# Kernel optimization log

Measured on AMD Instinct MI355X. Metric: run time of the kernel, lower is better.

## Reference

```python
import jax, jax.numpy as jnp
import numpy as np

BN_EPS = 1e-5


def _gin_layer(x, src, dst, n_nodes, W1, b1, W2, b2, gamma, beta):
    # GINConv with eps=0: z_i = x_i + sum_{(j->i) in E} x_j, then 2-layer MLP
    agg = jax.ops.segment_sum(x[src], dst, num_segments=n_nodes)  # [N, d]
    z = x + agg
    z = jax.nn.relu(z @ W1 + b1) @ W2 + b2
    # BatchNorm1d (training mode: biased batch statistics over node dim)
    mean = jnp.mean(z, axis=0)
    var = jnp.var(z, axis=0)
    z = (z - mean) * jax.lax.rsqrt(var + BN_EPS) * gamma + beta
    return jax.nn.relu(z)  # dropout p=0 -> identity


def setup_inputs() -> dict:
    key = jax.random.key(0)
    ks = jax.random.split(key, 8)
    N, E, D, L = 50000, 800000, 128, 2
    h = jax.random.normal(ks[0], (N, D), dtype=jnp.float32)
    edge_index = jax.random.randint(ks[1], (2, E), 0, N, dtype=jnp.int64)
    scale = 1.0 / np.sqrt(D)
    W1 = jax.random.normal(ks[2], (L, D, D), dtype=jnp.float32) * scale
    b1 = jax.random.normal(ks[3], (L, D), dtype=jnp.float32) * 0.01
    W2 = jax.random.normal(ks[4], (L, D, D), dtype=jnp.float32) * scale
    b2 = jax.random.normal(ks[5], (L, D), dtype=jnp.float32) * 0.01
    gamma = jnp.ones((L, D), dtype=jnp.float32)
    beta = jnp.zeros((L, D), dtype=jnp.float32)
    return {"h": h, "edge_index": edge_index, "W1": W1, "b1": b1,
            "W2": W2, "b2": b2, "gamma": gamma, "beta": beta}


def reference(h, edge_index, W1, b1, W2, b2, gamma, beta):
    src, dst = edge_index[0], edge_index[1]
    n_nodes = h.shape[0]
    n_layers = W1.shape[0]
    outs = []
    x = h
    for i in range(n_layers):
        x = _gin_layer(x, src, dst, n_nodes, W1[i], b1[i], W2[i], b2[i], gamma[i], beta[i])
        outs.append(x)
    return jnp.stack(outs)  # [L, N, D] == hs[1:]
```

## Files before the change

kernel.cpp:

```cpp
#include <hip/hip_runtime.h>

#define D 128
#define BN_EPS 1e-5f

typedef __attribute__((ext_vector_type(8))) short short8;
typedef __attribute__((ext_vector_type(4))) float f32x4;

__device__ inline unsigned short f2bf(float f) {
    union { float f; unsigned int u; } v; v.f = f;
    unsigned int u = v.u;
    unsigned int r = (u + 0x7FFFu + ((u >> 16) & 1u)) >> 16;
    return (unsigned short)r;
}

__device__ inline float bfbits2f(unsigned int bits) {
    union { unsigned int u; float f; } v; v.u = bits;
    return v.f;
}

__device__ inline float4 bf2f4(uint2 v) {
    float4 r;
    r.x = bfbits2f(v.x << 16);
    r.y = bfbits2f(v.x & 0xFFFF0000u);
    r.z = bfbits2f(v.y << 16);
    r.w = bfbits2f(v.y & 0xFFFF0000u);
    return r;
}

__global__ void hist_dst(const int* __restrict__ dst, int* __restrict__ cnt, int E) {
    int e = blockIdx.x * blockDim.x + threadIdx.x;
    if (e < E) atomicAdd(&cnt[dst[e]], 1);
}

__global__ void reduce_cnt(const int* __restrict__ cnt, int* __restrict__ bsum, int n) {
    __shared__ int s[256];
    int tid = threadIdx.x;
    int i = blockIdx.x * 256 + tid;
    s[tid] = (i < n) ? cnt[i] : 0;
    __syncthreads();
    for (int ofs = 128; ofs > 0; ofs >>= 1) {
        if (tid < ofs) s[tid] += s[tid + ofs];
        __syncthreads();
    }
    if (tid == 0) bsum[blockIdx.x] = s[0];
}

__global__ void scan_bsums(const int* __restrict__ bsum, int* __restrict__ blockOff,
                           int* __restrict__ offN, int nb) {
    __shared__ int s[256];
    int tid = threadIdx.x;
    int v = (tid < nb) ? bsum[tid] : 0;
    s[tid] = v;
    __syncthreads();
    for (int ofs = 1; ofs < 256; ofs <<= 1) {
        int t = (tid >= ofs) ? s[tid - ofs] : 0;
        __syncthreads();
        s[tid] += t;
        __syncthreads();
    }
    if (tid < nb) blockOff[tid] = s[tid] - v;
    if (tid == nb - 1) *offN = s[tid];
}

__global__ void scan_partial(const int* __restrict__ cnt, int* __restrict__ off,
                             int* __restrict__ cursor, const int* __restrict__ blockOff, int n) {
    __shared__ int s[256];
    int tid = threadIdx.x;
    int i = blockIdx.x * 256 + tid;
    int v = (i < n) ? cnt[i] : 0;
    s[tid] = v;
    __syncthreads();
    for (int ofs = 1; ofs < 256; ofs <<= 1) {
        int t = (tid >= ofs) ? s[tid - ofs] : 0;
        __syncthreads();
        s[tid] += t;
        __syncthreads();
    }
    if (i < n) {
        int o = blockOff[blockIdx.x] + s[tid] - v;
        off[i] = o;
        cursor[i] = o;
    }
}

__global__ void fill_csr(const int* __restrict__ src, const int* __restrict__ dst,
                         int* __restrict__ cursor, int* __restrict__ eidx, int E) {
    int e = blockIdx.x * blockDim.x + threadIdx.x;
    if (e >= E) return;
    int d = dst[e];
    int pos = atomicAdd(&cursor[d], 1);
    eidx[pos] = src[e];
}

__global__ void wprep(const float* __restrict__ W1, const float* __restrict__ W2,
                      unsigned short* __restrict__ Wt, int L) {
    int idx = blockIdx.x * 256 + threadIdx.x;
    int m = idx >> 14;
    int rem = idx & 16383;
    int c = rem >> 7, k = rem & 127;
    const float* W = (m < L) ? (W1 + (size_t)m * D * D) : (W2 + (size_t)(m - L) * D * D);
    Wt[(size_t)m * D * D + c * D + k] = f2bf(W[k * D + c]);
}

__global__ void x2bf(const float* __restrict__ x, unsigned short* __restrict__ xb, int n8) {
    int i = blockIdx.x * 256 + threadIdx.x;
    if (i >= n8) return;
    float4 a = reinterpret_cast<const float4*>(x)[2 * i];
    float4 b = reinterpret_cast<const float4*>(x)[2 * i + 1];
    uint4 o;
    o.x = (unsigned)f2bf(a.x) | ((unsigned)f2bf(a.y) << 16);
    o.y = (unsigned)f2bf(a.z) | ((unsigned)f2bf(a.w) << 16);
    o.z = (unsigned)f2bf(b.x) | ((unsigned)f2bf(b.y) << 16);
    o.w = (unsigned)f2bf(b.z) | ((unsigned)f2bf(b.w) << 16);
    reinterpret_cast<uint4*>(xb)[i] = o;
}

__global__ __launch_bounds__(256) void gather_bf(
        const unsigned short* __restrict__ xb, const int* __restrict__ off,
        const int* __restrict__ eidx, unsigned short* __restrict__ zb, int N) {
    int t = blockIdx.x * blockDim.x + threadIdx.x;
    int node = t >> 5;
    if (node >= N) return;
    int lane = t & 31;
    int beg = off[node], end = off[node + 1];
    float4 acc = bf2f4(*reinterpret_cast<const uint2*>(xb + (size_t)node * D + lane * 4));
    int e = beg;
    for (; e + 2 <= end; e += 2) {
        int s0 = eidx[e], s1 = eidx[e + 1];
        uint2 v0 = *reinterpret_cast<const uint2*>(xb + (size_t)s0 * D + lane * 4);
        uint2 v1 = *reinterpret_cast<const uint2*>(xb + (size_t)s1 * D + lane * 4);
        float4 f0 = bf2f4(v0), f1 = bf2f4(v1);
        acc.x += f0.x + f1.x; acc.y += f0.y + f1.y;
        acc.z += f0.z + f1.z; acc.w += f0.w + f1.w;
    }
    if (e < end) {
        int s0 = eidx[e];
        float4 f0 = bf2f4(*reinterpret_cast<const uint2*>(xb + (size_t)s0 * D + lane * 4));
        acc.x += f0.x; acc.y += f0.y; acc.z += f0.z; acc.w += f0.w;
    }
    uint2 o;
    o.x = (unsigned)f2bf(acc.x) | ((unsigned)f2bf(acc.y) << 16);
    o.y = (unsigned)f2bf(acc.z) | ((unsigned)f2bf(acc.w) << 16);
    *reinterpret_cast<uint2*>(zb + (size_t)node * D + lane * 4) = o;
}

__global__ __launch_bounds__(256) void gemm1_mfma(
        const unsigned short* __restrict__ A, const unsigned short* __restrict__ Wt,
        const float* __restrict__ bias, unsigned short* __restrict__ Out, int N) {
    __shared__ __align__(16) char sW[32768];
    const int tid = threadIdx.x;
    #pragma unroll
    for (int it = 0; it < 8; it++) {
        int idx = tid + it * 256;
        int row = idx >> 4, slot = idx & 15;
        uint4 v = *reinterpret_cast<const uint4*>(Wt + ((size_t)idx << 3));
        *reinterpret_cast<uint4*>(sW + row * 256 + ((slot * 16) ^ ((row & 7) << 4))) = v;
    }
    __syncthreads();

    const int lane = tid & 63, wv = tid >> 6;
    const int r0 = blockIdx.x * 64 + wv * 16;
    int arow = r0 + (lane & 15); if (arow >= N) arow = N - 1;
    const unsigned short* aptr = A + (size_t)arow * D + ((lane >> 4) << 3);

    f32x4 acc[8];
    #pragma unroll
    for (int ct = 0; ct < 8; ct++) {
        float b = bias[ct * 16 + (lane & 15)];
        acc[ct] = (f32x4){b, b, b, b};
    }
    #pragma unroll
    for (int ks = 0; ks < 4; ks++) {
        short8 a = *reinterpret_cast<const short8*>(aptr + ks * 32);
        #pragma unroll
        for (int ct = 0; ct < 8; ct++) {
            int rr = ct * 16 + (lane & 15);
            int kb = ks * 64 + ((lane >> 4) << 4);
            short8 bfr = *reinterpret_cast<const short8*>(sW + rr * 256 + (kb ^ ((rr & 7) << 4)));
            acc[ct] = __builtin_amdgcn_mfma_f32_16x16x32_bf16(a, bfr, acc[ct], 0, 0, 0);
        }
    }
    #pragma unroll
    for (int ct = 0; ct < 8; ct++) {
        #pragma unroll
        for (int r = 0; r < 4; r++) {
            int row = r0 + ((lane >> 4) << 2) + r;
            if (row < N)
                Out[(size_t)row * D + ct * 16 + (lane & 15)] = f2bf(fmaxf(acc[ct][r], 0.f));
        }
    }
}

__global__ __launch_bounds__(256) void gemm2_mfma(
        const unsigned short* __restrict__ A, const unsigned short* __restrict__ Wt,
        const float* __restrict__ bias, float* __restrict__ Out,
        float* __restrict__ gstats, int N) {
    __shared__ __align__(16) char sW[32768];
    __shared__ float sStat[2 * D];
    const int tid = threadIdx.x;
    if (tid < 2 * D) sStat[tid] = 0.f;
    #pragma unroll
    for (int it = 0; it < 8; it++) {
        int idx = tid + it * 256;
        int row = idx >> 4, slot = idx & 15;
        uint4 v = *reinterpret_cast<const uint4*>(Wt + ((size_t)idx << 3));
        *reinterpret_cast<uint4*>(sW + row * 256 + ((slot * 16) ^ ((row & 7) << 4))) = v;
    }
    __syncthreads();

    const int lane = tid & 63, wv = tid >> 6;
    const int r0 = blockIdx.x * 64 + wv * 16;
    int arow = r0 + (lane & 15); if (arow >= N) arow = N - 1;
    const unsigned short* aptr = A + (size_t)arow * D + ((lane >> 4) << 3);

    f32x4 acc[8];
    #pragma unroll
    for (int ct = 0; ct < 8; ct++) {
        float b = bias[ct * 16 + (lane & 15)];
        acc[ct] = (f32x4){b, b, b, b};
    }
    #pragma unroll
    for (int ks = 0; ks < 4; ks++) {
        short8 a = *reinterpret_cast<const short8*>(aptr + ks * 32);
        #pragma unroll
        for (int ct = 0; ct < 8; ct++) {
            int rr = ct * 16 + (lane & 15);
            int kb = ks * 64 + ((lane >> 4) << 4);
            short8 bfr = *reinterpret_cast<const short8*>(sW + rr * 256 + (kb ^ ((rr & 7) << 4)));
            acc[ct] = __builtin_amdgcn_mfma_f32_16x16x32_bf16(a, bfr, acc[ct], 0, 0, 0);
        }
    }
    #pragma unroll
    for (int ct = 0; ct < 8; ct++) {
        float s = 0.f, q = 0.f;
        #pragma unroll
        for (int r = 0; r < 4; r++) {
            int row = r0 + ((lane >> 4) << 2) + r;
            float v = acc[ct][r];
            if (row < N) {
                Out[(size_t)row * D + ct * 16 + (lane & 15)] = v;
                s += v; q += v * v;
            }
        }
        s += __shfl_xor(s, 16); q += __shfl_xor(q, 16);
        s += __shfl_xor(s, 32); q += __shfl_xor(q, 32);
        if (lane < 16) {
            atomicAdd(&sStat[ct * 16 + lane], s);
            atomicAdd(&sStat[D + ct * 16 + lane], q);
        }
    }
    __syncthreads();
    if (tid < 2 * D) atomicAdd(&gstats[tid], sStat[tid]);
}

__global__ void bn_relu_bf(float* __restrict__ y, unsigned short* __restrict__ xb,
                           const float* __restrict__ stats,
                           const float* __restrict__ gamma, const float* __restrict__ beta,
                           int N) {
    int i = blockIdx.x * blockDim.x + threadIdx.x;
    int n4 = N * D / 4;
    if (i >= n4) return;
    int c0 = (i << 2) & (D - 1);
    float4 v = reinterpret_cast<float4*>(y)[i];
    float o[4] = {v.x, v.y, v.z, v.w};
    float invN = 1.0f / (float)N;
    #pragma unroll
    for (int j = 0; j < 4; j++) {
        int c = c0 + j;
        float mean = stats[c] * invN;
        float var  = stats[D + c] * invN - mean * mean;
        float sc = rsqrtf(var + BN_EPS) * gamma[c];
        float t = (o[j] - mean) * sc + beta[c];
        o[j] = fmaxf(t, 0.f);
    }
    float4 r; r.x = o[0]; r.y = o[1]; r.z = o[2]; r.w = o[3];
    reinterpret_cast<float4*>(y)[i] = r;
    uint2 ob;
    ob.x = (unsigned)f2bf(o[0]) | ((unsigned)f2bf(o[1]) << 16);
    ob.y = (unsigned)f2bf(o[2]) | ((unsigned)f2bf(o[3]) << 16);
    reinterpret_cast<uint2*>(xb)[i] = ob;
}

extern "C" void kernel_launch(void* const* d_in, const int* in_sizes, int n_in,
                              void* d_out, int out_size, void* d_ws, size_t ws_size,
                              hipStream_t stream) {
    const float* h     = (const float*)d_in[0];
    const int*   ei    = (const int*)d_in[1];
    const float* W1    = (const float*)d_in[2];
    const float* b1    = (const float*)d_in[3];
    const float* W2    = (const float*)d_in[4];
    const float* b2    = (const float*)d_in[5];
    const float* gamma = (const float*)d_in[6];
    const float* beta  = (const float*)d_in[7];
    float* out = (float*)d_out;

    const int N = in_sizes[0] / D;
    const int E = in_sizes[1] / 2;
    const int L = in_sizes[2] / (D * D);
    const int nb = (N + 255) / 256;

    unsigned short* zb  = (unsigned short*)d_ws;
    unsigned short* xb  = zb + (size_t)N * D;
    unsigned short* Wt  = xb + (size_t)N * D;
    float* stats = (float*)(Wt + (size_t)2 * L * D * D);
    int* cnt      = (int*)(stats + (size_t)L * 2 * D);
    int* off      = cnt + N;
    int* cursor   = off + N + 1;
    int* bsum     = cursor + N;
    int* blockOff = bsum + nb;
    int* eidx     = blockOff + nb;

    const int* src = ei;
    const int* dst = ei + E;

    const int n4 = N * D / 4;
    const int n8 = N * D / 8;
    const int ewBlocks = (E + 255) / 256;
    const int gatherBlocks = (N * 32 + 255) / 256;
    const int gemmBlocks = (N + 63) / 64;
    const int bnBlocks = (n4 + 255) / 256;
    const int wprepBlocks = (2 * L * D * D) / 256;

    hipMemsetAsync(cnt, 0, N * sizeof(int), stream);
    hipMemsetAsync(stats, 0, (size_t)L * 2 * D * sizeof(float), stream);
    wprep<<<wprepBlocks, 256, 0, stream>>>(W1, W2, Wt, L);
    x2bf<<<(n8 + 255) / 256, 256, 0, stream>>>(h, xb, n8);

    hist_dst<<<ewBlocks, 256, 0, stream>>>(dst, cnt, E);
    reduce_cnt<<<nb, 256, 0, stream>>>(cnt, bsum, N);
    scan_bsums<<<1, 256, 0, stream>>>(bsum, blockOff, off + N, nb);
    scan_partial<<<nb, 256, 0, stream>>>(cnt, off, cursor, blockOff, N);
    fill_csr<<<ewBlocks, 256, 0, stream>>>(src, dst, cursor, eidx, E);

    for (int l = 0; l < L; l++) {
        float* y = out + (size_t)l * N * D;

        gather_bf<<<gatherBlocks, 256, 0, stream>>>(xb, off, eidx, zb, N);
        gemm1_mfma<<<gemmBlocks, 256, 0, stream>>>(zb, Wt + (size_t)l * D * D,
                                                   b1 + (size_t)l * D, zb, N);
        gemm2_mfma<<<gemmBlocks, 256, 0, stream>>>(zb, Wt + (size_t)(L + l) * D * D,
                                                   b2 + (size_t)l * D, y, stats + (size_t)l * 2 * D, N);
        bn_relu_bf<<<bnBlocks, 256, 0, stream>>>(y, xb, stats + (size_t)l * 2 * D,
                                                 gamma + (size_t)l * D, beta + (size_t)l * D, N);
    }
}
```

Baseline: 276.5 us.

## Record edge ranks during histogram and read GEMM weights directly from global memory

The histogram kernel now records each edge's atomic rank, so the CSR fill no longer needs a second pass of atomics on a cursor array and instead writes to off[dst]+rank. Both MFMA GEMM kernels drop the per-block LDS staging of the weight matrix. They read B fragments straight from global memory (served by cache) and process 32 rows per wave instead of 16, which reuses each B fragment across two MFMAs. This removes the shared-memory fill and barrier, halves the block count and raises register use. It also adds an E-sized rank buffer to the workspace.

```diff
diff --git a/kernel.cpp b/kernel.cpp
--- a/kernel.cpp
+++ b/kernel.cpp
@@ -27,9 +27,11 @@
     return r;
 }
 
-__global__ void hist_dst(const int* __restrict__ dst, int* __restrict__ cnt, int E) {
+__global__ void hist_rank(const int* __restrict__ dst, int* __restrict__ cnt,
+                          int* __restrict__ rank, int E) {
     int e = blockIdx.x * blockDim.x + threadIdx.x;
-    if (e < E) atomicAdd(&cnt[dst[e]], 1);
+    if (e >= E) return;
+    rank[e] = atomicAdd(&cnt[dst[e]], 1);
 }
 
 __global__ void reduce_cnt(const int* __restrict__ cnt, int* __restrict__ bsum, int n) {
@@ -63,7 +65,7 @@
 }
 
 __global__ void scan_partial(const int* __restrict__ cnt, int* __restrict__ off,
-                             int* __restrict__ cursor, const int* __restrict__ blockOff, int n) {
+                             const int* __restrict__ blockOff, int n) {
     __shared__ int s[256];
     int tid = threadIdx.x;
     int i = blockIdx.x * 256 + tid;
@@ -76,20 +78,15 @@
         s[tid] += t;
         __syncthreads();
     }
-    if (i < n) {
-        int o = blockOff[blockIdx.x] + s[tid] - v;
-        off[i] = o;
-        cursor[i] = o;
-    }
-}
-
-__global__ void fill_csr(const int* __restrict__ src, const int* __restrict__ dst,
-                         int* __restrict__ cursor, int* __restrict__ eidx, int E) {
+    if (i < n) off[i] = blockOff[blockIdx.x] + s[tid] - v;
+}
+
+__global__ void fill2(const int* __restrict__ src, const int* __restrict__ dst,
+                      const int* __restrict__ rank, const int* __restrict__ off,
+                      int* __restrict__ eidx, int E) {
     int e = blockIdx.x * blockDim.x + threadIdx.x;
     if (e >= E) return;
-    int d = dst[e];
-    int pos = atomicAdd(&cursor[d], 1);
-    eidx[pos] = src[e];
+    eidx[off[dst[e]] + rank[e]] = src[e];
 }
 
 __global__ void wprep(const float* __restrict__ W1, const float* __restrict__ W2,
@@ -147,46 +144,46 @@
 __global__ __launch_bounds__(256) void gemm1_mfma(
         const unsigned short* __restrict__ A, const unsigned short* __restrict__ Wt,
         const float* __restrict__ bias, unsigned short* __restrict__ Out, int N) {
-    __shared__ __align__(16) char sW[32768];
     const int tid = threadIdx.x;
-    #pragma unroll
-    for (int it = 0; it < 8; it++) {
-        int idx = tid + it * 256;
-        int row = idx >> 4, slot = idx & 15;
-        uint4 v = *reinterpret_cast<const uint4*>(Wt + ((size_t)idx << 3));
-        *reinterpret_cast<uint4*>(sW + row * 256 + ((slot * 16) ^ ((row & 7) << 4))) = v;
-    }
-    __syncthreads();
-
     const int lane = tid & 63, wv = tid >> 6;
-    const int r0 = blockIdx.x * 64 + wv * 16;
-    int arow = r0 + (lane & 15); if (arow >= N) arow = N - 1;
-    const unsigned short* aptr = A + (size_t)arow * D + ((lane >> 4) << 3);
-
-    f32x4 acc[8];
+    const int r0 = blockIdx.x * 128 + wv * 32;
+    const int koff = (lane >> 4) << 3;
+    const int col = lane & 15;
+
+    int ar0 = r0 + col;       if (ar0 >= N) ar0 = N - 1;
+    int ar1 = r0 + 16 + col;  if (ar1 >= N) ar1 = N - 1;
+    const unsigned short* ap0 = A + (size_t)ar0 * D + koff;
+    const unsigned short* ap1 = A + (size_t)ar1 * D + koff;
+    const unsigned short* wp  = Wt + (size_t)col * D + koff;
+
+    f32x4 acc[2][8];
     #pragma unroll
     for (int ct = 0; ct < 8; ct++) {
-        float b = bias[ct * 16 + (lane & 15)];
-        acc[ct] = (f32x4){b, b, b, b};
+        float b = bias[ct * 16 + col];
+        acc[0][ct] = (f32x4){b, b, b, b};
+        acc[1][ct] = (f32x4){b, b, b, b};
     }
     #pragma unroll
     for (int ks = 0; ks < 4; ks++) {
-        short8 a = *reinterpret_cast<const short8*>(aptr + ks * 32);
+        short8 a0 = *reinterpret_cast<const short8*>(ap0 + ks * 32);
+        short8 a1 = *reinterpret_cast<const short8*>(ap1 + ks * 32);
         #pragma unroll
         for (int ct = 0; ct < 8; ct++) {
-            int rr = ct * 16 + (lane & 15);
-            int kb = ks * 64 + ((lane >> 4) << 4);
-            short8 bfr = *reinterpret_cast<const short8*>(sW + rr * 256 + (kb ^ ((rr & 7) << 4)));
-            acc[ct] = __builtin_amdgcn_mfma_f32_16x16x32_bf16(a, bfr, acc[ct], 0, 0, 0);
-        }
-    }
-    #pragma unroll
-    for (int ct = 0; ct < 8; ct++) {
+            short8 bfr = *reinterpret_cast<const short8*>(wp + (size_t)ct * 16 * D + ks * 32);
+            acc[0][ct] = __builtin_amdgcn_mfma_f32_16x16x32_bf16(a0, bfr, acc[0][ct], 0, 0, 0);
+            acc[1][ct] = __builtin_amdgcn_mfma_f32_16x16x32_bf16(a1, bfr, acc[1][ct], 0, 0, 0);
+        }
+    }
+    #pragma unroll
+    for (int t = 0; t < 2; t++) {
         #pragma unroll
-        for (int r = 0; r < 4; r++) {
-            int row = r0 + ((lane >> 4) << 2) + r;
-            if (row < N)
-                Out[(size_t)row * D + ct * 16 + (lane & 15)] = f2bf(fmaxf(acc[ct][r], 0.f));
+        for (int ct = 0; ct < 8; ct++) {
+            #pragma unroll
+            for (int r = 0; r < 4; r++) {
+                int row = r0 + t * 16 + ((lane >> 4) << 2) + r;
+                if (row < N)
+                    Out[(size_t)row * D + ct * 16 + col] = f2bf(fmaxf(acc[t][ct][r], 0.f));
+            }
         }
     }
 }
@@ -195,51 +192,53 @@
         const unsigned short* __restrict__ A, const unsigned short* __restrict__ Wt,
         const float* __restrict__ bias, float* __restrict__ Out,
         float* __restrict__ gstats, int N) {
-    __shared__ __align__(16) char sW[32768];
     __shared__ float sStat[2 * D];
     const int tid = threadIdx.x;
     if (tid < 2 * D) sStat[tid] = 0.f;
-    #pragma unroll
-    for (int it = 0; it < 8; it++) {
-        int idx = tid + it * 256;
-        int row = idx >> 4, slot = idx & 15;
-        uint4 v = *reinterpret_cast<const uint4*>(Wt + ((size_t)idx << 3));
-        *reinterpret_cast<uint4*>(sW + row * 256 + ((slot * 16) ^ ((row & 7) << 4))) = v;
-    }
     __syncthreads();
 
     const int lane = tid & 63, wv = tid >> 6;
-    const int r0 = blockIdx.x * 64 + wv * 16;
-    int arow = r0 + (lane & 15); if (arow >= N) arow = N - 1;
-    const unsigned short* aptr = A + (size_t)arow * D + ((lane >> 4) << 3);
-
-    f32x4 acc[8];
+    const int r0 = blockIdx.x * 128 + wv * 32;
+    const int koff = (lane >> 4) << 3;
+    const int col = lane & 15;
+
+    int ar0 = r0 + col;       if (ar0 >= N) ar0 = N - 1;
+    int ar1 = r0 + 16 + col;  if (ar1 >= N) ar1 = N - 1;
+    const unsigned short* ap0 = A + (size_t)ar0 * D + koff;
+    const unsigned short* ap1 = A + (size_t)ar1 * D + koff;
+    const unsigned short* wp  = Wt + (size_t)col * D + koff;
+
+    f32x4 acc[2][8];
     #pragma unroll
     for (int ct = 0; ct < 8; ct++) {
-        float b = bias[ct * 16 + (lane & 15)];
-        acc[ct] = (f32x4){b, b, b, b};
+        float b = bias[ct * 16 + col];
+        acc[0][ct] = (f32x4){b, b, b, b};
+        acc[1][ct] = (f32x4){b, b, b, b};
     }
     #pragma unroll
     for (int ks = 0; ks < 4; ks++) {
-        short8 a = *reinterpret_cast<const short8*>(aptr + ks * 32);
+        short8 a0 = *reinterpret_cast<const short8*>(ap0 + ks * 32);
+        short8 a1 = *reinterpret_cast<const short8*>(ap1 + ks * 32);
         #pragma unroll
         for (int ct = 0; ct < 8; ct++) {
-            int rr = ct * 16 + (lane & 15);
-            int kb = ks * 64 + ((lane >> 4) << 4);
-            short8 bfr = *reinterpret_cast<const short8*>(sW + rr * 256 + (kb ^ ((rr & 7) << 4)));
-            acc[ct] = __builtin_amdgcn_mfma_f32_16x16x32_bf16(a, bfr, acc[ct], 0, 0, 0);
+            short8 bfr = *reinterpret_cast<const short8*>(wp + (size_t)ct * 16 * D + ks * 32);
+            acc[0][ct] = __builtin_amdgcn_mfma_f32_16x16x32_bf16(a0, bfr, acc[0][ct], 0, 0, 0);
+            acc[1][ct] = __builtin_amdgcn_mfma_f32_16x16x32_bf16(a1, bfr, acc[1][ct], 0, 0, 0);
         }
     }
     #pragma unroll
     for (int ct = 0; ct < 8; ct++) {
         float s = 0.f, q = 0.f;
         #pragma unroll
-        for (int r = 0; r < 4; r++) {
-            int row = r0 + ((lane >> 4) << 2) + r;
-            float v = acc[ct][r];
-            if (row < N) {
-                Out[(size_t)row * D + ct * 16 + (lane & 15)] = v;
-                s += v; q += v * v;
+        for (int t = 0; t < 2; t++) {
+            #pragma unroll
+            for (int r = 0; r < 4; r++) {
+                int row = r0 + t * 16 + ((lane >> 4) << 2) + r;
+                float v = acc[t][ct][r];
+                if (row < N) {
+                    Out[(size_t)row * D + ct * 16 + col] = v;
+                    s += v; q += v * v;
+                }
             }
         }
         s += __shfl_xor(s, 16); q += __shfl_xor(q, 16);
@@ -305,10 +304,10 @@
     float* stats = (float*)(Wt + (size_t)2 * L * D * D);
     int* cnt      = (int*)(stats + (size_t)L * 2 * D);
     int* off      = cnt + N;
-    int* cursor   = off + N + 1;
-    int* bsum     = cursor + N;
+    int* bsum     = off + N + 1;
     int* blockOff = bsum + nb;
-    int* eidx     = blockOff + nb;
+    int* rank     = blockOff + nb;
+    int* eidx     = rank + E;
 
     const int* src = ei;
     const int* dst = ei + E;
@@ -317,7 +316,7 @@
     const int n8 = N * D / 8;
     const int ewBlocks = (E + 255) / 256;
     const int gatherBlocks = (N * 32 + 255) / 256;
-    const int gemmBlocks = (N + 63) / 64;
+    const int gemmBlocks = (N + 127) / 128;
     const int bnBlocks = (n4 + 255) / 256;
     const int wprepBlocks = (2 * L * D * D) / 256;
 
@@ -326,11 +325,11 @@
     wprep<<<wprepBlocks, 256, 0, stream>>>(W1, W2, Wt, L);
     x2bf<<<(n8 + 255) / 256, 256, 0, stream>>>(h, xb, n8);
 
-    hist_dst<<<ewBlocks, 256, 0, stream>>>(dst, cnt, E);
+    hist_rank<<<ewBlocks, 256, 0, stream>>>(dst, cnt, rank, E);
     reduce_cnt<<<nb, 256, 0, stream>>>(cnt, bsum, N);
     scan_bsums<<<1, 256, 0, stream>>>(bsum, blockOff, off + N, nb);
-    scan_partial<<<nb, 256, 0, stream>>>(cnt, off, cursor, blockOff, N);
-    fill_csr<<<ewBlocks, 256, 0, stream>>>(src, dst, cursor, eidx, E);
+    scan_partial<<<nb, 256, 0, stream>>>(cnt, off, blockOff, N);
+    fill2<<<ewBlocks, 256, 0, stream>>>(src, dst, rank, off, eidx, E);
 
     for (int l = 0; l < L; l++) {
         float* y = out + (size_t)l * N * D;
```

After: 244.2 us. 1.13x faster.
